# Optimization experiments

Hardware: AMD Instinct MI355X
Metric: run time of the kernel (lower is better)

The kernel has to match this reference:

```python
import jax, jax.numpy as jnp
import numpy as np

B, S, D, H = 8, 2048, 1024, 64

def setup_inputs() -> dict:
    key = jax.random.key(0)
    k1, k2, k3, k4 = jax.random.split(key, 4)
    idx = jax.random.normal(k1, (B, S, D), dtype=jnp.float32)
    # nn.Linear(D, H, bias=False) weights, stored as [D, H] for x @ W
    Wk = jax.random.normal(k2, (D, H), dtype=jnp.float32) * (1.0 / np.sqrt(D))
    Wq = jax.random.normal(k3, (D, H), dtype=jnp.float32) * (1.0 / np.sqrt(D))
    Wv = jax.random.normal(k4, (D, H), dtype=jnp.float32) * (1.0 / np.sqrt(D))
    return {"idx": idx, "Wk": Wk, "Wq": Wq, "Wv": Wv}

def reference(idx, Wk, Wq, Wv):
    b, s, d = idx.shape
    k = idx @ Wk  # [b, s, h]
    q = idx @ Wq
    v = idx @ Wv
    # NOTE: original scales by embedding_dim**-0.5, not head_size**-0.5
    wei = jnp.einsum('bqh,bkh->bqk', q, k) * (d ** -0.5)
    causal = jnp.tril(jnp.ones((s, s), dtype=bool))
    wei = jnp.where(causal, wei, -jnp.inf)
    attn = jax.nn.softmax(wei, axis=-1)  # dropout p=0.0 -> identity
    return jnp.einsum('bqk,bkh->bqh', attn, v)
```

## Files before the change

### kernel.cpp

```cpp
#include <hip/hip_runtime.h>

typedef __attribute__((ext_vector_type(8))) short short8;
typedef __attribute__((ext_vector_type(4))) short short4v;
typedef __attribute__((ext_vector_type(4))) float f32x4;

#define MFMA_16x16x32_BF16(A, B, C) __builtin_amdgcn_mfma_f32_16x16x32_bf16(A, B, C, 0, 0, 0)

__device__ __forceinline__ unsigned short f2bf(float x) {
    unsigned int u = __builtin_bit_cast(unsigned int, x);
    u = (u + 0x7FFFu + ((u >> 16) & 1u)) >> 16;
    return (unsigned short)u;
}

__global__ __launch_bounds__(256) void wconv_kernel(const float* __restrict__ Wk,
                                                    const float* __restrict__ Wq,
                                                    const float* __restrict__ Wv,
                                                    unsigned short* __restrict__ Wt) {
    const int n = blockIdx.x;
    const float* W = (n < 64) ? Wk : (n < 128) ? Wq : Wv;
    const int col = n & 63;
    const int sw = (n & 7) << 3;
    for (int k = threadIdx.x; k < 1024; k += 256) {
        const int kd = (k & ~56) | ((k ^ sw) & 56);
        Wt[(size_t)n * 1024 + kd] = f2bf(W[(size_t)k * 64 + col]);
    }
}

__global__ __launch_bounds__(512, 4) void proj_kernel(const float* __restrict__ X,
                                                      const unsigned short* __restrict__ Wt,
                                                      unsigned short* __restrict__ Kb,
                                                      unsigned short* __restrict__ Qb,
                                                      unsigned short* __restrict__ Vtg) {
    __shared__ __attribute__((aligned(16))) unsigned short Wl[2][192 * 64];
    __shared__ __attribute__((aligned(16))) unsigned short Al[2][32 * 72];
    const int t = threadIdx.x;
    const int w = t >> 6, lane = t & 63, lr = lane & 15, g = lane >> 4;
    const int rw = w >> 2, cw = w & 3;
    const int r0 = blockIdx.x * 32;

    f32x4 acc[3] = {};

    const int ar = t >> 4, ac = (t & 15) * 4;
    const float* xsrc = X + (size_t)(r0 + ar) * 1024 + ac;

    float4 fly = *(const float4*)xsrc;
    uint2 aw;
    aw.x = (unsigned)f2bf(fly.x) | ((unsigned)f2bf(fly.y) << 16);
    aw.y = (unsigned)f2bf(fly.z) | ((unsigned)f2bf(fly.w) << 16);
    *(uint2*)&Al[0][ar * 72 + ac] = aw;
#pragma unroll
    for (int i = 0; i < 3; ++i) {
        const int q = t + 512 * i;
        const unsigned short* src = Wt + (size_t)(q >> 3) * 1024 + (q & 7) * 8;
        __builtin_amdgcn_global_load_lds((const __attribute__((address_space(1))) void*)src,
                                         (__attribute__((address_space(3))) void*)&Wl[0][q * 8],
                                         16, 0, 0);
    }
    __builtin_amdgcn_sched_barrier(0);
    fly = *(const float4*)(xsrc + 64);
    asm volatile("s_waitcnt vmcnt(1) lgkmcnt(0)" ::: "memory");
    __builtin_amdgcn_s_barrier();

    for (int t16 = 0; t16 < 16; ++t16) {
        const int cur = t16 & 1;
        if (t16 < 15) {
            aw.x = (unsigned)f2bf(fly.x) | ((unsigned)f2bf(fly.y) << 16);
            aw.y = (unsigned)f2bf(fly.z) | ((unsigned)f2bf(fly.w) << 16);
            *(uint2*)&Al[cur ^ 1][ar * 72 + ac] = aw;
            const int k1 = (t16 + 1) * 64;
#pragma unroll
            for (int i = 0; i < 3; ++i) {
                const int q = t + 512 * i;
                const unsigned short* src = Wt + (size_t)(q >> 3) * 1024 + k1 + (q & 7) * 8;
                __builtin_amdgcn_global_load_lds((const __attribute__((address_space(1))) void*)src,
                                                 (__attribute__((address_space(3))) void*)&Wl[cur ^ 1][q * 8],
                                                 16, 0, 0);
            }
            __builtin_amdgcn_sched_barrier(0);
            const int anext = (t16 + 2 < 15) ? (t16 + 2) : 15;
            fly = *(const float4*)(xsrc + anext * 64);
        }

        short8 af[2];
        af[0] = *(const short8*)&Al[cur][(16 * rw + lr) * 72 + 8 * g];
        af[1] = *(const short8*)&Al[cur][(16 * rw + lr) * 72 + 32 + 8 * g];
#pragma unroll
        for (int c = 0; c < 3; ++c) {
            const int row = 48 * cw + 16 * c + lr;
#pragma unroll
            for (int sub = 0; sub < 2; ++sub) {
                const int cs = (4 * sub + g) ^ (lr & 7);
                short8 wf = *(const short8*)&Wl[cur][row * 64 + cs * 8];
                acc[c] = MFMA_16x16x32_BF16(af[sub], wf, acc[c]);
            }
        }
        asm volatile("s_waitcnt vmcnt(1) lgkmcnt(0)" ::: "memory");
        __builtin_amdgcn_s_barrier();
    }

    const int bb = r0 >> 11;
    const int sb0 = (r0 & 2047) + 16 * rw + 4 * g;
    const int row = r0 + 16 * rw + 4 * g;
#pragma unroll
    for (int i = 0; i < 3; ++i) {
        const int cg = cw * 3 + i;
        if (cg < 4) {
#pragma unroll
            for (int r = 0; r < 4; ++r)
                Kb[(size_t)(row + r) * 64 + 16 * cg + lr] = f2bf(acc[i][r]);
        } else if (cg < 8) {
#pragma unroll
            for (int r = 0; r < 4; ++r)
                Qb[(size_t)(row + r) * 64 + 16 * (cg - 4) + lr] = f2bf(acc[i][r]);
        } else {
            const int h = 16 * (cg - 8) + lr;
            uint2 e;
            e.x = (unsigned)f2bf(acc[i][0]) | ((unsigned)f2bf(acc[i][1]) << 16);
            e.y = (unsigned)f2bf(acc[i][2]) | ((unsigned)f2bf(acc[i][3]) << 16);
            *(uint2*)(Vtg + (size_t)bb * 64 * 2048 + (size_t)h * 2048 + sb0) = e;
        }
    }
}

__global__ __launch_bounds__(1024, 4) void attn_kernel(const unsigned short* __restrict__ Kb,
                                                       const unsigned short* __restrict__ Qb,
                                                       const unsigned short* __restrict__ Vtg,
                                                       float* __restrict__ out) {
    __shared__ __attribute__((aligned(16))) float Pacc[16][32][68];
    __shared__ float Pml[2][16][32];

    const int t = threadIdx.x;
    const int w = t >> 6, lane = t & 63;
    const int lr = lane & 15, g = lane >> 4;
    const int p = blockIdx.x, b = blockIdx.y;
    const int band = w >> 3, wi = w & 7;
    const int nb = band ? (p + 1) : (64 - p);
    const int q0 = band ? p * 32 : (63 - p) * 32;
    const size_t rowbase = (size_t)b * 2048;
    const size_t vbase = (size_t)b * 64 * 2048;
    const float NEG_INF = -__builtin_inff();
    const float SCALE2 = 0.03125f * 1.4426950408889634f;

    short8 qf[2][2];
#pragma unroll
    for (int sub = 0; sub < 2; ++sub)
#pragma unroll
        for (int hh = 0; hh < 2; ++hh)
            qf[sub][hh] = *(const short8*)(Qb + (rowbase + q0 + 16 * sub + lr) * 64 + 32 * hh + 8 * g);

    f32x4 acc[2][4] = {};
    float m2[2] = {NEG_INF, NEG_INF};
    float ls[2] = {0.f, 0.f};

    const int s0 = (wi * nb) >> 3, s1 = ((wi + 1) * nb) >> 3;

    for (int s = s0; s < s1; ++s) {
        const int kv0 = s * 32;
        short8 kf[2][2];
#pragma unroll
        for (int f = 0; f < 2; ++f)
#pragma unroll
            for (int hh = 0; hh < 2; ++hh)
                kf[f][hh] = *(const short8*)(Kb + (rowbase + kv0 + 16 * f + lr) * 64 + 32 * hh + 8 * g);
        short8 vf[4];
#pragma unroll
        for (int fh = 0; fh < 4; ++fh) {
            const unsigned short* vp = Vtg + vbase + (size_t)(16 * fh + lr) * 2048 + kv0 + 4 * g;
            short4v v0 = *(const short4v*)vp;
            short4v v1 = *(const short4v*)(vp + 16);
            short8 vv;
            vv[0] = v0[0]; vv[1] = v0[1]; vv[2] = v0[2]; vv[3] = v0[3];
            vv[4] = v1[0]; vv[5] = v1[1]; vv[6] = v1[2]; vv[7] = v1[3];
            vf[fh] = vv;
        }
#pragma unroll
        for (int sub = 0; sub < 2; ++sub) {
            f32x4 sv[2];
#pragma unroll
            for (int f = 0; f < 2; ++f) {
                f32x4 x = {};
                x = MFMA_16x16x32_BF16(kf[f][0], qf[sub][0], x);
                x = MFMA_16x16x32_BF16(kf[f][1], qf[sub][1], x);
                sv[f] = x;
            }
            const int q = q0 + 16 * sub + lr;
            float pvv[8], tmax = NEG_INF;
#pragma unroll
            for (int f = 0; f < 2; ++f)
#pragma unroll
                for (int r = 0; r < 4; ++r) {
                    int kp = kv0 + 16 * f + 4 * g + r;
                    float sc = sv[f][r] * SCALE2;
                    sc = (kp <= q) ? sc : NEG_INF;
                    pvv[4 * f + r] = sc;
                    tmax = fmaxf(tmax, sc);
                }
            tmax = fmaxf(tmax, __shfl_xor(tmax, 16));
            tmax = fmaxf(tmax, __shfl_xor(tmax, 32));
            float mnew = fmaxf(m2[sub], tmax);
            float alpha = exp2f(m2[sub] - mnew);
            float psum = 0.f;
            short8 pf;
#pragma unroll
            for (int e = 0; e < 8; ++e) {
                float pe = exp2f(pvv[e] - mnew);
                psum += pe;
                pf[e] = (short)f2bf(pe);
            }
            psum += __shfl_xor(psum, 16);
            psum += __shfl_xor(psum, 32);
            ls[sub] = ls[sub] * alpha + psum;
            m2[sub] = mnew;
#pragma unroll
            for (int fh = 0; fh < 4; ++fh) {
                acc[sub][fh][0] *= alpha; acc[sub][fh][1] *= alpha;
                acc[sub][fh][2] *= alpha; acc[sub][fh][3] *= alpha;
                acc[sub][fh] = MFMA_16x16x32_BF16(vf[fh], pf, acc[sub][fh]);
            }
        }
    }

    {
        const int slot = band * 8 + wi;
#pragma unroll
        for (int sub = 0; sub < 2; ++sub) {
#pragma unroll
            for (int fh = 0; fh < 4; ++fh)
                *(f32x4*)&Pacc[slot][16 * sub + lr][16 * fh + 4 * g] = acc[sub][fh];
            if (g == 0) {
                Pml[0][slot][16 * sub + lr] = m2[sub];
                Pml[1][slot][16 * sub + lr] = ls[sub];
            }
        }
    }
    __syncthreads();

    {
        const int tb = t >> 9, t2 = t & 511;
        const int qq = t2 & 31, hb = (t2 >> 5) * 4;
        float mw[8], M = NEG_INF;
#pragma unroll
        for (int wv = 0; wv < 8; ++wv) {
            mw[wv] = Pml[0][tb * 8 + wv][qq];
            M = fmaxf(M, mw[wv]);
        }
        float wgt[8], L = 0.f;
#pragma unroll
        for (int wv = 0; wv < 8; ++wv) {
            wgt[wv] = exp2f(mw[wv] - M);
            L += wgt[wv] * Pml[1][tb * 8 + wv][qq];
        }
        f32x4 o = {};
#pragma unroll
        for (int wv = 0; wv < 8; ++wv)
            o += wgt[wv] * *(const f32x4*)&Pacc[tb * 8 + wv][qq][hb];
        o *= (1.f / L);
        const int qb = tb ? p * 32 : (63 - p) * 32;
        *(f32x4*)(out + (rowbase + qb + qq) * 64 + hb) = o;
    }
}

extern "C" void kernel_launch(void* const* d_in, const int* in_sizes, int n_in,
                              void* d_out, int out_size, void* d_ws, size_t ws_size,
                              hipStream_t stream) {
    const float* X  = (const float*)d_in[0];
    const float* Wk = (const float*)d_in[1];
    const float* Wq = (const float*)d_in[2];
    const float* Wv = (const float*)d_in[3];

    unsigned short* Wt  = (unsigned short*)d_ws;
    unsigned short* Kb  = Wt + 192 * 1024;
    unsigned short* Qb  = Kb + 16384 * 64;
    unsigned short* Vtg = Qb + 16384 * 64;
    float* out = (float*)d_out;

    wconv_kernel<<<dim3(192), dim3(256), 0, stream>>>(Wk, Wq, Wv, Wt);
    proj_kernel<<<dim3(512), dim3(512), 0, stream>>>(X, Wt, Kb, Qb, Vtg);
    attn_kernel<<<dim3(32, 8), dim3(1024), 0, stream>>>(Kb, Qb, Vtg, out);
}
```

Before: 54.97 us.

## Permute V layout for 16-byte loads and halve attention block to 8 waves

```diff
diff --git a/kernel.cpp b/kernel.cpp
--- a/kernel.cpp
+++ b/kernel.cpp
@@ -1,7 +1,6 @@
 #include <hip/hip_runtime.h>
 
 typedef __attribute__((ext_vector_type(8))) short short8;
-typedef __attribute__((ext_vector_type(4))) short short4v;
 typedef __attribute__((ext_vector_type(4))) float f32x4;
 
 #define MFMA_16x16x32_BF16(A, B, C) __builtin_amdgcn_mfma_f32_16x16x32_bf16(A, B, C, 0, 0, 0)
@@ -30,7 +29,7 @@
                                                       const unsigned short* __restrict__ Wt,
                                                       unsigned short* __restrict__ Kb,
                                                       unsigned short* __restrict__ Qb,
-                                                      unsigned short* __restrict__ Vtg) {
+                                                      unsigned short* __restrict__ Vt2) {
     __shared__ __attribute__((aligned(16))) unsigned short Wl[2][192 * 64];
     __shared__ __attribute__((aligned(16))) unsigned short Al[2][32 * 72];
     const int t = threadIdx.x;
@@ -99,7 +98,6 @@
     }
 
     const int bb = r0 >> 11;
-    const int sb0 = (r0 & 2047) + 16 * rw + 4 * g;
     const int row = r0 + 16 * rw + 4 * g;
 #pragma unroll
     for (int i = 0; i < 3; ++i) {
@@ -117,15 +115,16 @@
             uint2 e;
             e.x = (unsigned)f2bf(acc[i][0]) | ((unsigned)f2bf(acc[i][1]) << 16);
             e.y = (unsigned)f2bf(acc[i][2]) | ((unsigned)f2bf(acc[i][3]) << 16);
-            *(uint2*)(Vtg + (size_t)bb * 64 * 2048 + (size_t)h * 2048 + sb0) = e;
-        }
-    }
-}
-
-__global__ __launch_bounds__(1024, 4) void attn_kernel(const unsigned short* __restrict__ Kb,
-                                                       const unsigned short* __restrict__ Qb,
-                                                       const unsigned short* __restrict__ Vtg,
-                                                       float* __restrict__ out) {
+            *(uint2*)(Vt2 + (size_t)bb * 64 * 2048 + (size_t)h * 2048
+                      + ((r0 & 2047) >> 5) * 32 + g * 8 + 4 * rw) = e;
+        }
+    }
+}
+
+__global__ __launch_bounds__(512, 2) void attn_kernel(const unsigned short* __restrict__ Kb,
+                                                      const unsigned short* __restrict__ Qb,
+                                                      const unsigned short* __restrict__ Vt2,
+                                                      float* __restrict__ out) {
     __shared__ __attribute__((aligned(16))) float Pacc[16][32][68];
     __shared__ float Pml[2][16][32];
 
@@ -133,46 +132,42 @@
     const int w = t >> 6, lane = t & 63;
     const int lr = lane & 15, g = lane >> 4;
     const int p = blockIdx.x, b = blockIdx.y;
-    const int band = w >> 3, wi = w & 7;
-    const int nb = band ? (p + 1) : (64 - p);
-    const int q0 = band ? p * 32 : (63 - p) * 32;
+    const int nhi = 64 - p;
+    const int q0h = (63 - p) * 32, q0l = p * 32;
     const size_t rowbase = (size_t)b * 2048;
     const size_t vbase = (size_t)b * 64 * 2048;
     const float NEG_INF = -__builtin_inff();
     const float SCALE2 = 0.03125f * 1.4426950408889634f;
 
-    short8 qf[2][2];
+    short8 qfH[2][2], qfL[2][2];
 #pragma unroll
     for (int sub = 0; sub < 2; ++sub)
 #pragma unroll
-        for (int hh = 0; hh < 2; ++hh)
-            qf[sub][hh] = *(const short8*)(Qb + (rowbase + q0 + 16 * sub + lr) * 64 + 32 * hh + 8 * g);
-
-    f32x4 acc[2][4] = {};
-    float m2[2] = {NEG_INF, NEG_INF};
-    float ls[2] = {0.f, 0.f};
-
-    const int s0 = (wi * nb) >> 3, s1 = ((wi + 1) * nb) >> 3;
-
-    for (int s = s0; s < s1; ++s) {
-        const int kv0 = s * 32;
-        short8 kf[2][2];
+        for (int hh = 0; hh < 2; ++hh) {
+            qfH[sub][hh] = *(const short8*)(Qb + (rowbase + q0h + 16 * sub + lr) * 64 + 32 * hh + 8 * g);
+            qfL[sub][hh] = *(const short8*)(Qb + (rowbase + q0l + 16 * sub + lr) * 64 + 32 * hh + 8 * g);
+        }
+
+    f32x4 accH[2][4] = {}, accL[2][4] = {};
+    float mH[2] = {NEG_INF, NEG_INF}, mL[2] = {NEG_INF, NEG_INF};
+    float lH[2] = {0.f, 0.f}, lL[2] = {0.f, 0.f};
+
+    const int s0 = (w * 65) >> 3, s1 = ((w + 1) * 65) >> 3;
+
+    auto loadS = [&](int kv0, short8 (&kf)[2][2], short8 (&vf)[4]) {
 #pragma unroll
         for (int f = 0; f < 2; ++f)
 #pragma unroll
             for (int hh = 0; hh < 2; ++hh)
                 kf[f][hh] = *(const short8*)(Kb + (rowbase + kv0 + 16 * f + lr) * 64 + 32 * hh + 8 * g);
-        short8 vf[4];
-#pragma unroll
-        for (int fh = 0; fh < 4; ++fh) {
-            const unsigned short* vp = Vtg + vbase + (size_t)(16 * fh + lr) * 2048 + kv0 + 4 * g;
-            short4v v0 = *(const short4v*)vp;
-            short4v v1 = *(const short4v*)(vp + 16);
-            short8 vv;
-            vv[0] = v0[0]; vv[1] = v0[1]; vv[2] = v0[2]; vv[3] = v0[3];
-            vv[4] = v1[0]; vv[5] = v1[1]; vv[6] = v1[2]; vv[7] = v1[3];
-            vf[fh] = vv;
-        }
+#pragma unroll
+        for (int fh = 0; fh < 4; ++fh)
+            vf[fh] = *(const short8*)(Vt2 + vbase + (size_t)(16 * fh + lr) * 2048 + (kv0 >> 5) * 32 + 8 * g);
+    };
+
+    auto comp = [&](int kv0, int q0, const short8 (&qf)[2][2],
+                    const short8 (&kf)[2][2], const short8 (&vf)[4],
+                    f32x4 (&acc)[2][4], float (&m2)[2], float (&ls)[2]) {
 #pragma unroll
         for (int sub = 0; sub < 2; ++sub) {
             f32x4 sv[2];
@@ -218,10 +213,44 @@
                 acc[sub][fh] = MFMA_16x16x32_BF16(vf[fh], pf, acc[sub][fh]);
             }
         }
-    }
+    };
+
+    short8 kfA[2][2], vfA[4], kfB[2][2], vfB[4];
 
     {
-        const int slot = band * 8 + wi;
+        const int e = (s1 < nhi) ? s1 : nhi;
+        int s = s0;
+        for (; s + 1 < e; s += 2) {
+            loadS(s * 32, kfA, vfA);
+            loadS((s + 1) * 32, kfB, vfB);
+            comp(s * 32, q0h, qfH, kfA, vfA, accH, mH, lH);
+            comp((s + 1) * 32, q0h, qfH, kfB, vfB, accH, mH, lH);
+        }
+        if (s < e) {
+            loadS(s * 32, kfA, vfA);
+            comp(s * 32, q0h, qfH, kfA, vfA, accH, mH, lH);
+        }
+    }
+    {
+        int s = (s0 > nhi) ? s0 : nhi;
+        for (; s + 1 < s1; s += 2) {
+            loadS((s - nhi) * 32, kfA, vfA);
+            loadS((s + 1 - nhi) * 32, kfB, vfB);
+            comp((s - nhi) * 32, q0l, qfL, kfA, vfA, accL, mL, lL);
+            comp((s + 1 - nhi) * 32, q0l, qfL, kfB, vfB, accL, mL, lL);
+        }
+        if (s < s1) {
+            loadS((s - nhi) * 32, kfA, vfA);
+            comp((s - nhi) * 32, q0l, qfL, kfA, vfA, accL, mL, lL);
+        }
+    }
+
+#pragma unroll
+    for (int bnd = 0; bnd < 2; ++bnd) {
+        const f32x4 (&acc)[2][4] = bnd ? accL : accH;
+        const float (&m2)[2] = bnd ? mL : mH;
+        const float (&ls)[2] = bnd ? lL : lH;
+        const int slot = bnd * 8 + w;
 #pragma unroll
         for (int sub = 0; sub < 2; ++sub) {
 #pragma unroll
@@ -236,8 +265,8 @@
     __syncthreads();
 
     {
-        const int tb = t >> 9, t2 = t & 511;
-        const int qq = t2 & 31, hb = (t2 >> 5) * 4;
+        const int tb = t >> 8, t2 = t & 255;
+        const int qq = t2 & 31, hb = (t2 >> 5) * 8;
         float mw[8], M = NEG_INF;
 #pragma unroll
         for (int wv = 0; wv < 8; ++wv) {
@@ -250,13 +279,20 @@
             wgt[wv] = exp2f(mw[wv] - M);
             L += wgt[wv] * Pml[1][tb * 8 + wv][qq];
         }
-        f32x4 o = {};
-#pragma unroll
-        for (int wv = 0; wv < 8; ++wv)
-            o += wgt[wv] * *(const f32x4*)&Pacc[tb * 8 + wv][qq][hb];
-        o *= (1.f / L);
-        const int qb = tb ? p * 32 : (63 - p) * 32;
-        *(f32x4*)(out + (rowbase + qb + qq) * 64 + hb) = o;
+        f32x4 o0 = {}, o1 = {};
+#pragma unroll
+        for (int wv = 0; wv < 8; ++wv) {
+            f32x4 a0 = *(const f32x4*)&Pacc[tb * 8 + wv][qq][hb];
+            f32x4 a1 = *(const f32x4*)&Pacc[tb * 8 + wv][qq][hb + 4];
+            o0 += wgt[wv] * a0;
+            o1 += wgt[wv] * a1;
+        }
+        const float invL = 1.f / L;
+        o0 *= invL; o1 *= invL;
+        const int q0 = tb ? q0l : q0h;
+        float* op = out + (rowbase + q0 + qq) * 64 + hb;
+        *(f32x4*)op = o0;
+        *(f32x4*)(op + 4) = o1;
     }
 }
 
@@ -271,10 +307,10 @@
     unsigned short* Wt  = (unsigned short*)d_ws;
     unsigned short* Kb  = Wt + 192 * 1024;
     unsigned short* Qb  = Kb + 16384 * 64;
-    unsigned short* Vtg = Qb + 16384 * 64;
+    unsigned short* Vt2 = Qb + 16384 * 64;
     float* out = (float*)d_out;
 
     wconv_kernel<<<dim3(192), dim3(256), 0, stream>>>(Wk, Wq, Wv, Wt);
-    proj_kernel<<<dim3(512), dim3(512), 0, stream>>>(X, Wt, Kb, Qb, Vtg);
-    attn_kernel<<<dim3(32, 8), dim3(1024), 0, stream>>>(Kb, Qb, Vtg, out);
-}
+    proj_kernel<<<dim3(512), dim3(512), 0, stream>>>(X, Wt, Kb, Qb, Vt2);
+    attn_kernel<<<dim3(32, 8), dim3(512), 0, stream>>>(Kb, Qb, Vt2, out);
+}
```

Result: faster. 49.03 us, median of 3 (-10.8%).
